# Optimization experiments

Measured on AMD Instinct MI355X. Metric: run time of the kernel, lower is better.

Reference implementation:

```python
import jax, jax.numpy as jnp
import numpy as np
import math

N_HEAD = 16
N_KV_HEAD = 4
N_EMBD = 2048
HEAD_DIM = N_EMBD // N_HEAD  # 128
SCALE = 1.0 / math.sqrt(HEAD_DIM)
B, T = 2, 2048


def setup_inputs() -> dict:
    key = jax.random.key(0)
    ks = jax.random.split(key, 5)
    s = 0.02
    x = jax.random.normal(ks[0], (B, T, N_EMBD), dtype=jnp.float32)
    wq = jax.random.normal(ks[1], (N_EMBD, N_EMBD), dtype=jnp.float32) * s
    wk = jax.random.normal(ks[2], (N_KV_HEAD * HEAD_DIM, N_EMBD), dtype=jnp.float32) * s
    wv = jax.random.normal(ks[3], (N_KV_HEAD * HEAD_DIM, N_EMBD), dtype=jnp.float32) * s
    wo = jax.random.normal(ks[4], (N_EMBD, N_EMBD), dtype=jnp.float32) * s
    return {"x": x, "wq": wq, "wk": wk, "wv": wv, "wo": wo}


def _forward(x, wq, wk, wv, wo):
    b, t, _ = x.shape
    # Linear layers: y = x @ W.T  (torch Linear weight is (out,in))
    q = (x @ wq.T).reshape(b, t, N_HEAD, HEAD_DIM).transpose(0, 2, 1, 3)      # (B,H,T,D)
    k = (x @ wk.T).reshape(b, t, N_KV_HEAD, HEAD_DIM).transpose(0, 2, 1, 3)  # (B,Hkv,T,D)
    v = (x @ wv.T).reshape(b, t, N_KV_HEAD, HEAD_DIM).transpose(0, 2, 1, 3)
    groups = N_HEAD // N_KV_HEAD
    k = jnp.repeat(k, groups, axis=1)  # repeat_interleave over head dim -> (B,H,T,D)
    v = jnp.repeat(v, groups, axis=1)
    # Causal mask: True above diagonal (masked-out positions)
    mask = jnp.triu(jnp.ones((t, t), dtype=bool), k=1)[None, None]  # (1,1,T,T)
    scores = jnp.einsum('bhqd,bhkd->bhqk', q, k) * SCALE
    scores = jnp.where(mask, -jnp.inf, scores)
    attn = jax.nn.softmax(scores, axis=-1)
    attn = jnp.where(mask, 0.0, attn)
    y = jnp.einsum('bhqk,bhkd->bhqd', attn, v)       # (B,H,T,D)
    y = y.transpose(0, 2, 1, 3).reshape(b, t, N_EMBD)
    return y @ wo.T


def reference(x, wq, wk, wv, wo):
    return _forward(x, wq, wk, wv, wo)
```

## Files before the change

### kernel.cpp

```cpp
#include <hip/hip_runtime.h>
#include <cstdint>
#include <cstddef>

typedef __bf16 bf16_t;
typedef __bf16 bf16x8 __attribute__((ext_vector_type(8)));
typedef __bf16 bf16x4 __attribute__((ext_vector_type(4)));
typedef float f32x4 __attribute__((ext_vector_type(4)));

#define GL2LDS16(gptr, lptr)                                                   \
  __builtin_amdgcn_global_load_lds(                                            \
      (__attribute__((address_space(1))) void*)(gptr),                         \
      (__attribute__((address_space(3))) void*)(lptr), 16, 0, 0)

__device__ __forceinline__ float fast_exp2(float x) {
  float r;
  asm volatile("v_exp_f32 %0, %1" : "=v"(r) : "v"(x));
  return r;
}

#define BATCH 2
#define T_SEQ 2048
#define NH 16
#define NKV 4
#define HD 128
#define EMB 2048
#define KVDIM (NKV * HD)
#define MROWS (BATCH * T_SEQ)

__global__ void cvt_all(const float4* __restrict__ x,  const float4* __restrict__ wq,
                        const float4* __restrict__ wk, const float4* __restrict__ wv,
                        const float4* __restrict__ wo,
                        bf16x4* __restrict__ xb,  bf16x4* __restrict__ wqb,
                        bf16x4* __restrict__ wkb, bf16x4* __restrict__ wvb,
                        bf16x4* __restrict__ wob) {
  const int blk = blockIdx.x;
  const float4* src;
  bf16x4* dst;
  int base;
  if (blk < 8192)       { src = x;  dst = xb;  base = blk; }
  else if (blk < 12288) { src = wq; dst = wqb; base = blk - 8192; }
  else if (blk < 13312) { src = wk; dst = wkb; base = blk - 12288; }
  else if (blk < 14336) { src = wv; dst = wvb; base = blk - 13312; }
  else                  { src = wo; dst = wob; base = blk - 14336; }
  const int i = base * 256 + threadIdx.x;
  const float4 v = src[i];
  dst[i] = bf16x4{(__bf16)v.x, (__bf16)v.y, (__bf16)v.z, (__bf16)v.w};
}

#define BK8 64
#define NT8 (EMB / BK8)

__global__ __launch_bounds__(512, 2)
void gemm_qkv8(const bf16_t* __restrict__ A,
               const bf16_t* __restrict__ Wq, const bf16_t* __restrict__ Wk,
               const bf16_t* __restrict__ Wv,
               bf16_t* __restrict__ Qb, bf16_t* __restrict__ Kb,
               bf16_t* __restrict__ Vt, float qalpha)
{
  __shared__ bf16_t lds[2][512 * 64];

  const int tid  = threadIdx.x;
  const int lane = tid & 63;
  const int wv   = tid >> 6;
  const int l15  = lane & 15;
  const int lq   = lane >> 4;

  const int bid0 = blockIdx.x;
  const int bid  = (bid0 & 7) * 24 + (bid0 >> 3);
  const int mt = bid / 12, nt = bid % 12;
  const int m0 = mt * 256;

  const bf16_t* Bmat; int ncol0, seg;
  if (nt < 8)       { Bmat = Wq; ncol0 = nt * 256;        seg = 0; }
  else if (nt < 10) { Bmat = Wk; ncol0 = (nt - 8) * 256;  seg = 1; }
  else              { Bmat = Wv; ncol0 = (nt - 10) * 256; seg = 2; }

  const int wm = (wv >> 2) * 128;
  const int wn = (wv & 3) * 64;

  f32x4 acc[8][4] = {};

  auto stage = [&](int dbuf, int tsrc, int h) {
    const int k0 = tsrc * BK8;
    const bf16_t* src = (h < 2) ? A : Bmat;
    const int rbase = (h < 2) ? (m0 + h * 128) : (ncol0 + (h - 2) * 128);
    bf16_t* dst = &lds[dbuf][h * 8192];
#pragma unroll
    for (int r = 0; r < 2; ++r) {
      const int c = r * 512 + tid;
      const int row = c >> 3, p = c & 7;
      const int sb = p ^ (row & 7);
      GL2LDS16(src + (size_t)(rbase + row) * EMB + k0 + sb * 8, dst + c * 8);
    }
  };

  stage(0, 0, 0); stage(0, 0, 1); stage(0, 0, 2); stage(0, 0, 3);
  stage(1, 1, 2); stage(1, 1, 0); stage(1, 1, 3);
  asm volatile("s_waitcnt vmcnt(6)" ::: "memory");
  __builtin_amdgcn_s_barrier();

  bf16x8 a[4][2], b[4][2];

#pragma unroll 1
  for (int tt = 0; tt < NT8; tt += 2) {
#pragma unroll
    for (int u = 0; u < 2; ++u) {
      const int t   = tt + u;
      const int cur = u;
      const int nxt = u ^ 1;
      const int tn1 = (t + 1 < NT8) ? t + 1 : NT8 - 1;
      const int tn2 = (t + 2 < NT8) ? t + 2 : NT8 - 1;

#pragma unroll
      for (int i = 0; i < 4; ++i) {
        const int row = wm + i * 16 + l15;
#pragma unroll
        for (int ks = 0; ks < 2; ++ks)
          a[i][ks] = *(const bf16x8*)&lds[cur][row * 64 + (((ks * 4 + lq) ^ (row & 7)) * 8)];
      }
#pragma unroll
      for (int j = 0; j < 2; ++j) {
        const int row = 256 + wn + j * 16 + l15;
#pragma unroll
        for (int ks = 0; ks < 2; ++ks)
          b[j][ks] = *(const bf16x8*)&lds[cur][row * 64 + (((ks * 4 + lq) ^ (row & 7)) * 8)];
      }
      stage(nxt, tn1, 1);
      __builtin_amdgcn_s_barrier();
      __builtin_amdgcn_s_setprio(1);
#pragma unroll
      for (int ks = 0; ks < 2; ++ks)
#pragma unroll
        for (int i = 0; i < 4; ++i)
#pragma unroll
          for (int j = 0; j < 2; ++j)
            acc[i][j] = __builtin_amdgcn_mfma_f32_16x16x32_bf16(a[i][ks], b[j][ks], acc[i][j], 0, 0, 0);
      __builtin_amdgcn_s_setprio(0);
      __builtin_amdgcn_s_barrier();

#pragma unroll
      for (int j = 2; j < 4; ++j) {
        const int row = 256 + wn + j * 16 + l15;
#pragma unroll
        for (int ks = 0; ks < 2; ++ks)
          b[j][ks] = *(const bf16x8*)&lds[cur][row * 64 + (((ks * 4 + lq) ^ (row & 7)) * 8)];
      }
      __builtin_amdgcn_s_barrier();
      __builtin_amdgcn_s_setprio(1);
#pragma unroll
      for (int ks = 0; ks < 2; ++ks)
#pragma unroll
        for (int i = 0; i < 4; ++i)
#pragma unroll
          for (int j = 2; j < 4; ++j)
            acc[i][j] = __builtin_amdgcn_mfma_f32_16x16x32_bf16(a[i][ks], b[j][ks], acc[i][j], 0, 0, 0);
      __builtin_amdgcn_s_setprio(0);
      __builtin_amdgcn_s_barrier();

#pragma unroll
      for (int i = 0; i < 4; ++i) {
        const int row = wm + (4 + i) * 16 + l15;
#pragma unroll
        for (int ks = 0; ks < 2; ++ks)
          a[i][ks] = *(const bf16x8*)&lds[cur][row * 64 + (((ks * 4 + lq) ^ (row & 7)) * 8)];
      }
      stage(cur, tn2, 2);
      __builtin_amdgcn_s_barrier();
      __builtin_amdgcn_s_setprio(1);
#pragma unroll
      for (int ks = 0; ks < 2; ++ks)
#pragma unroll
        for (int i = 0; i < 4; ++i)
#pragma unroll
          for (int j = 2; j < 4; ++j)
            acc[4 + i][j] = __builtin_amdgcn_mfma_f32_16x16x32_bf16(a[i][ks], b[j][ks], acc[4 + i][j], 0, 0, 0);
      __builtin_amdgcn_s_setprio(0);
      __builtin_amdgcn_s_barrier();

      stage(cur, tn2, 0);
      stage(cur, tn2, 3);
      __builtin_amdgcn_s_barrier();
      __builtin_amdgcn_s_setprio(1);
#pragma unroll
      for (int ks = 0; ks < 2; ++ks)
#pragma unroll
        for (int i = 0; i < 4; ++i)
#pragma unroll
          for (int j = 0; j < 2; ++j)
            acc[4 + i][j] = __builtin_amdgcn_mfma_f32_16x16x32_bf16(a[i][ks], b[j][ks], acc[4 + i][j], 0, 0, 0);
      __builtin_amdgcn_s_setprio(0);
      asm volatile("s_waitcnt vmcnt(6)" ::: "memory");
      __builtin_amdgcn_s_barrier();
    }
  }
  asm volatile("s_waitcnt vmcnt(0)" ::: "memory");

  if (seg == 0) {
#pragma unroll
    for (int i = 0; i < 8; ++i) {
      const int rbase = m0 + wm + i * 16 + lq * 4;
#pragma unroll
      for (int j = 0; j < 4; ++j) {
        const int col = ncol0 + wn + j * 16 + l15;
#pragma unroll
        for (int r = 0; r < 4; ++r)
          Qb[(size_t)(rbase + r) * EMB + col] = (bf16_t)(acc[i][j][r] * qalpha);
      }
    }
  } else if (seg == 1) {
#pragma unroll
    for (int i = 0; i < 8; ++i) {
      const int rbase = m0 + wm + i * 16 + lq * 4;
#pragma unroll
      for (int j = 0; j < 4; ++j) {
        const int col = ncol0 + wn + j * 16 + l15;
#pragma unroll
        for (int r = 0; r < 4; ++r)
          Kb[(size_t)(rbase + r) * KVDIM + col] = (bf16_t)acc[i][j][r];
      }
    }
  } else {
    const int bb = m0 >> 11;
    const int mloc0 = (m0 & 2047) + wm + lq * 4;
#pragma unroll
    for (int i = 0; i < 8; ++i) {
      const int mloc = mloc0 + i * 16;
#pragma unroll
      for (int j = 0; j < 4; ++j) {
        const int d = ncol0 + wn + j * 16 + l15;
        *(bf16x4*)(Vt + (size_t)(bb * KVDIM + d) * T_SEQ + mloc) =
            bf16x4{(__bf16)acc[i][j][0], (__bf16)acc[i][j][1],
                   (__bf16)acc[i][j][2], (__bf16)acc[i][j][3]};
      }
    }
  }
}

__global__ __launch_bounds__(256, 2)
void gemm_out(const bf16_t* __restrict__ A, const bf16_t* __restrict__ Bm,
              float* __restrict__ C, int M, int N, int K)
{
  __shared__ bf16_t As[128 * 64];
  __shared__ bf16_t Bs[128 * 64];

  const int tid  = threadIdx.x;
  const int lane = tid & 63;
  const int wv   = tid >> 6;
  const int m0 = blockIdx.y * 128;
  const int n0 = blockIdx.x * 128;
  const int wm = (wv >> 1) * 64;
  const int wn = (wv & 1) * 64;
  const int l15 = lane & 15;
  const int lq  = lane >> 4;

  f32x4 acc[4][4] = {};
  const int srow = tid >> 3;
  const int scol = (tid & 7) * 8;

  for (int k0 = 0; k0 < K; k0 += 64) {
#pragma unroll
    for (int r = 0; r < 4; ++r) {
      const int row = r * 32 + srow;
      GL2LDS16(A + (size_t)(m0 + row) * K + k0 + scol, As + row * 64 + scol);
    }
#pragma unroll
    for (int r = 0; r < 4; ++r) {
      const int row = r * 32 + srow;
      GL2LDS16(Bm + (size_t)(n0 + row) * K + k0 + scol, Bs + row * 64 + scol);
    }
    __syncthreads();

#pragma unroll
    for (int ks = 0; ks < 2; ++ks) {
      const int kc = ks * 32 + lq * 8;
      bf16x8 af[4], bf[4];
#pragma unroll
      for (int i = 0; i < 4; ++i)
        af[i] = *(const bf16x8*)(As + (wm + i * 16 + l15) * 64 + kc);
#pragma unroll
      for (int j = 0; j < 4; ++j)
        bf[j] = *(const bf16x8*)(Bs + (wn + j * 16 + l15) * 64 + kc);
#pragma unroll
      for (int i = 0; i < 4; ++i)
#pragma unroll
        for (int j = 0; j < 4; ++j)
          acc[i][j] = __builtin_amdgcn_mfma_f32_16x16x32_bf16(af[i], bf[j], acc[i][j], 0, 0, 0);
    }
    __syncthreads();
  }

#pragma unroll
  for (int i = 0; i < 4; ++i) {
    const int rbase = m0 + wm + i * 16 + lq * 4;
#pragma unroll
    for (int j = 0; j < 4; ++j) {
      const int col = n0 + wn + j * 16 + l15;
#pragma unroll
      for (int r = 0; r < 4; ++r)
        C[(size_t)(rbase + r) * N + col] = acc[i][j][r];
    }
  }
}

#define PSTR 72

__global__ __launch_bounds__(256, 2)
void attn_fwd(const bf16_t* __restrict__ Q, const bf16_t* __restrict__ Kg,
              const bf16_t* __restrict__ Vt, bf16_t* __restrict__ Y)
{
  __shared__ bf16_t Ks[2][64 * 128];
  __shared__ bf16_t Vs[2][128 * 64];
  __shared__ bf16_t Ps[4][16 * PSTR];

  const int tid  = threadIdx.x;
  const int lane = tid & 63;
  const int wv   = tid >> 6;
  const int l15  = lane & 15;
  const int lq   = lane >> 4;
  const int h  = blockIdx.y;
  const int b  = blockIdx.z;
  const int hkv = h >> 2;
  bf16_t* Psw = Ps[wv];

  auto stage = [&](int kt, int bufsel) {
    const int base_t = b * T_SEQ + kt * 64;
#pragma unroll
    for (int r = 0; r < 4; ++r) {
      const int c = r * 256 + tid;
      const int row = c >> 4, p = c & 15;
      const int sb = p ^ (row & 7);
      GL2LDS16(Kg + (size_t)(base_t + row) * KVDIM + hkv * HD + sb * 8,
               &Ks[bufsel][c * 8]);
    }
#pragma unroll
    for (int r = 0; r < 4; ++r) {
      const int c = r * 256 + tid;
      const int row = c >> 3, p = c & 7;
      const int sb = p ^ (row & 7);
      GL2LDS16(Vt + (size_t)(b * KVDIM + hkv * HD + row) * T_SEQ + kt * 64 + sb * 8,
               &Vs[bufsel][c * 8]);
    }
  };

#pragma unroll 1
  for (int ph = 0; ph < 2; ++ph) {
    const int qt = ph ? blockIdx.x : (31 - blockIdx.x);
    const int q0 = qt * 64;
    const int nkt = qt + 1;
    const int qabs = q0 + wv * 16 + l15;

    bf16x8 qf[4];
    {
      const bf16_t* qp = Q + ((size_t)(b * T_SEQ + qabs) * NH + h) * HD + lq * 8;
#pragma unroll
      for (int ds = 0; ds < 4; ++ds)
        qf[ds] = *(const bf16x8*)(qp + ds * 32);
    }

    float l_part = 0.f;
    f32x4 o[8];
#pragma unroll
    for (int nb = 0; nb < 8; ++nb) o[nb] = f32x4{0.f, 0.f, 0.f, 0.f};

    __syncthreads();
    stage(0, 0);

    for (int kt = 0; kt < nkt; ++kt) {
      const int cur = kt & 1;
      __syncthreads();
      if (kt + 1 < nkt) stage(kt + 1, cur ^ 1);

      f32x4 s[4];
#pragma unroll
      for (int nb = 0; nb < 4; ++nb) {
        s[nb] = f32x4{0.f, 0.f, 0.f, 0.f};
        const int row = nb * 16 + l15;
        const int r7  = row & 7;
#pragma unroll
        for (int ds = 0; ds < 4; ++ds) {
          const bf16x8 kf = *(const bf16x8*)&Ks[cur][row * 128 + (((ds * 4 + lq) ^ r7) * 8)];
          s[nb] = __builtin_amdgcn_mfma_f32_16x16x32_bf16(kf, qf[ds], s[nb], 0, 0, 0);
        }
      }

      const bool dia = (kt == nkt - 1);
#pragma unroll
      for (int nb = 0; nb < 4; ++nb) {
        const int kvb = kt * 64 + nb * 16 + lq * 4;
        float p0, p1, p2, p3;
        if (dia) {
          p0 = (kvb + 0 <= qabs) ? fast_exp2(s[nb][0]) : 0.f;
          p1 = (kvb + 1 <= qabs) ? fast_exp2(s[nb][1]) : 0.f;
          p2 = (kvb + 2 <= qabs) ? fast_exp2(s[nb][2]) : 0.f;
          p3 = (kvb + 3 <= qabs) ? fast_exp2(s[nb][3]) : 0.f;
        } else {
          p0 = fast_exp2(s[nb][0]);
          p1 = fast_exp2(s[nb][1]);
          p2 = fast_exp2(s[nb][2]);
          p3 = fast_exp2(s[nb][3]);
        }
        l_part += (p0 + p1) + (p2 + p3);
        *(bf16x4*)(Psw + l15 * PSTR + nb * 16 + lq * 4) =
            bf16x4{(__bf16)p0, (__bf16)p1, (__bf16)p2, (__bf16)p3};
      }

      asm volatile("s_waitcnt lgkmcnt(0)" ::: "memory");

#pragma unroll
      for (int ks = 0; ks < 2; ++ks) {
        const bf16x8 pf = *(const bf16x8*)(Psw + l15 * PSTR + ks * 32 + lq * 8);
#pragma unroll
        for (int nb = 0; nb < 8; ++nb) {
          const int row = nb * 16 + l15;
          const bf16x8 vf = *(const bf16x8*)&Vs[cur][row * 64 + (((ks * 4 + lq) ^ (row & 7)) * 8)];
          o[nb] = __builtin_amdgcn_mfma_f32_16x16x32_bf16(vf, pf, o[nb], 0, 0, 0);
        }
      }
    }

    float lt = l_part;
    lt += __shfl_xor(lt, 16);
    lt += __shfl_xor(lt, 32);
    const float inv = 1.f / lt;
    bf16_t* yp = Y + ((size_t)(b * T_SEQ + qabs) * NH + h) * HD + lq * 4;
#pragma unroll
    for (int nb = 0; nb < 8; ++nb) {
      *(bf16x4*)(yp + nb * 16) = bf16x4{(__bf16)(o[nb][0] * inv), (__bf16)(o[nb][1] * inv),
                                        (__bf16)(o[nb][2] * inv), (__bf16)(o[nb][3] * inv)};
    }
  }
}

extern "C" void kernel_launch(void* const* d_in, const int* in_sizes, int n_in,
                              void* d_out, int out_size, void* d_ws, size_t ws_size,
                              hipStream_t stream) {
  const float* x  = (const float*)d_in[0];
  const float* wq = (const float*)d_in[1];
  const float* wk = (const float*)d_in[2];
  const float* wv = (const float*)d_in[3];
  const float* wo = (const float*)d_in[4];
  float* out = (float*)d_out;

  const size_t n_x  = (size_t)MROWS * EMB;
  const size_t n_wq = (size_t)EMB * EMB;
  const size_t n_wk = (size_t)KVDIM * EMB;

  bf16_t* xb  = (bf16_t*)d_ws;
  bf16_t* wqb = xb  + n_x;
  bf16_t* wkb = wqb + n_wq;
  bf16_t* wvb = wkb + n_wk;
  bf16_t* wob = wvb + n_wk;
  bf16_t* Qb  = wob + n_wq;
  bf16_t* Kb  = Qb + (size_t)MROWS * EMB;
  bf16_t* Vtb = Kb + (size_t)MROWS * KVDIM;
  bf16_t* Yb  = Vtb + (size_t)MROWS * KVDIM;

  dim3 blk(256);

  cvt_all<<<dim3(18432), blk, 0, stream>>>(
      (const float4*)x, (const float4*)wq, (const float4*)wk, (const float4*)wv, (const float4*)wo,
      (bf16x4*)xb, (bf16x4*)wqb, (bf16x4*)wkb, (bf16x4*)wvb, (bf16x4*)wob);

  const float qalpha = 0.08838834764831845f * 1.4426950408889634f;
  gemm_qkv8<<<dim3(192), dim3(512), 0, stream>>>(xb, wqb, wkb, wvb,
                                                 Qb, Kb, Vtb, qalpha);

  attn_fwd<<<dim3(16, NH, BATCH), blk, 0, stream>>>(Qb, Kb, Vtb, Yb);

  gemm_out<<<dim3(EMB / 128, MROWS / 128), blk, 0, stream>>>(Yb, wob, out, MROWS, EMB, EMB);
}
```

Before: 278.9 us.

## Fuse all stages into one persistent kernel with grid-wide atomic barriers

Replaces the four launches (convert, QKV GEMM, attention, output GEMM) with one persistent kernel of 256 blocks that separates the phases with a software grid barrier built on an atomic counter. The goal is to remove launch overhead and inter-kernel gaps. In exchange, occupancy drops to one 512-thread block per CU with a large shared buffer, and the QKV phase uses only 192 of the 256 blocks. The attention and output GEMM work is remapped onto two 256-thread groups per block, and correctness relies on all blocks being resident at once.

```diff
diff --git a/kernel.cpp b/kernel.cpp
--- a/kernel.cpp
+++ b/kernel.cpp
@@ -27,406 +27,442 @@
 #define KVDIM (NKV * HD)
 #define MROWS (BATCH * T_SEQ)
 
-__global__ void cvt_all(const float4* __restrict__ x,  const float4* __restrict__ wq,
-                        const float4* __restrict__ wk, const float4* __restrict__ wv,
-                        const float4* __restrict__ wo,
-                        bf16x4* __restrict__ xb,  bf16x4* __restrict__ wqb,
-                        bf16x4* __restrict__ wkb, bf16x4* __restrict__ wvb,
-                        bf16x4* __restrict__ wob) {
-  const int blk = blockIdx.x;
-  const float4* src;
-  bf16x4* dst;
-  int base;
-  if (blk < 8192)       { src = x;  dst = xb;  base = blk; }
-  else if (blk < 12288) { src = wq; dst = wqb; base = blk - 8192; }
-  else if (blk < 13312) { src = wk; dst = wkb; base = blk - 12288; }
-  else if (blk < 14336) { src = wv; dst = wvb; base = blk - 13312; }
-  else                  { src = wo; dst = wob; base = blk - 14336; }
-  const int i = base * 256 + threadIdx.x;
-  const float4 v = src[i];
-  dst[i] = bf16x4{(__bf16)v.x, (__bf16)v.y, (__bf16)v.z, (__bf16)v.w};
-}
-
 #define BK8 64
 #define NT8 (EMB / BK8)
-
-__global__ __launch_bounds__(512, 2)
-void gemm_qkv8(const bf16_t* __restrict__ A,
-               const bf16_t* __restrict__ Wq, const bf16_t* __restrict__ Wk,
-               const bf16_t* __restrict__ Wv,
-               bf16_t* __restrict__ Qb, bf16_t* __restrict__ Kb,
-               bf16_t* __restrict__ Vt, float qalpha)
+#define PSTR 72
+#define GRIDB 256
+
+#define ATTN_GRP_BYTES 74752
+#define SMEM_BYTES 149504
+
+__device__ __forceinline__ void gbar(unsigned long long* cnt) {
+  __syncthreads();
+  if (threadIdx.x == 0) {
+    unsigned long long old = __hip_atomic_fetch_add(
+        cnt, 1ULL, __ATOMIC_ACQ_REL, __HIP_MEMORY_SCOPE_AGENT);
+    const unsigned long long tgt = (old / GRIDB + 1) * GRIDB;
+    while (__hip_atomic_load(cnt, __ATOMIC_ACQUIRE,
+                             __HIP_MEMORY_SCOPE_AGENT) < tgt)
+      __builtin_amdgcn_s_sleep(2);
+  }
+  __syncthreads();
+}
+
+__global__ __launch_bounds__(512, 1)
+void fused_all(const float* __restrict__ x,  const float* __restrict__ wq,
+               const float* __restrict__ wk, const float* __restrict__ wv,
+               const float* __restrict__ wo, float* __restrict__ out,
+               bf16_t* __restrict__ xb,  bf16_t* __restrict__ wqb,
+               bf16_t* __restrict__ wkb, bf16_t* __restrict__ wvb,
+               bf16_t* __restrict__ wob,
+               bf16_t* __restrict__ Qb,  bf16_t* __restrict__ Kb,
+               bf16_t* __restrict__ Vt,  bf16_t* __restrict__ Yb,
+               unsigned long long* __restrict__ cnt, float qalpha)
 {
-  __shared__ bf16_t lds[2][512 * 64];
-
-  const int tid  = threadIdx.x;
-  const int lane = tid & 63;
-  const int wv   = tid >> 6;
-  const int l15  = lane & 15;
-  const int lq   = lane >> 4;
-
-  const int bid0 = blockIdx.x;
-  const int bid  = (bid0 & 7) * 24 + (bid0 >> 3);
-  const int mt = bid / 12, nt = bid % 12;
-  const int m0 = mt * 256;
-
-  const bf16_t* Bmat; int ncol0, seg;
-  if (nt < 8)       { Bmat = Wq; ncol0 = nt * 256;        seg = 0; }
-  else if (nt < 10) { Bmat = Wk; ncol0 = (nt - 8) * 256;  seg = 1; }
-  else              { Bmat = Wv; ncol0 = (nt - 10) * 256; seg = 2; }
-
-  const int wm = (wv >> 2) * 128;
-  const int wn = (wv & 3) * 64;
-
-  f32x4 acc[8][4] = {};
-
-  auto stage = [&](int dbuf, int tsrc, int h) {
-    const int k0 = tsrc * BK8;
-    const bf16_t* src = (h < 2) ? A : Bmat;
-    const int rbase = (h < 2) ? (m0 + h * 128) : (ncol0 + (h - 2) * 128);
-    bf16_t* dst = &lds[dbuf][h * 8192];
-#pragma unroll
-    for (int r = 0; r < 2; ++r) {
-      const int c = r * 512 + tid;
-      const int row = c >> 3, p = c & 7;
-      const int sb = p ^ (row & 7);
-      GL2LDS16(src + (size_t)(rbase + row) * EMB + k0 + sb * 8, dst + c * 8);
-    }
-  };
-
-  stage(0, 0, 0); stage(0, 0, 1); stage(0, 0, 2); stage(0, 0, 3);
-  stage(1, 1, 2); stage(1, 1, 0); stage(1, 1, 3);
-  asm volatile("s_waitcnt vmcnt(6)" ::: "memory");
-  __builtin_amdgcn_s_barrier();
-
-  bf16x8 a[4][2], b[4][2];
-
-#pragma unroll 1
-  for (int tt = 0; tt < NT8; tt += 2) {
-#pragma unroll
-    for (int u = 0; u < 2; ++u) {
-      const int t   = tt + u;
-      const int cur = u;
-      const int nxt = u ^ 1;
-      const int tn1 = (t + 1 < NT8) ? t + 1 : NT8 - 1;
-      const int tn2 = (t + 2 < NT8) ? t + 2 : NT8 - 1;
-
-#pragma unroll
-      for (int i = 0; i < 4; ++i) {
-        const int row = wm + i * 16 + l15;
-#pragma unroll
-        for (int ks = 0; ks < 2; ++ks)
-          a[i][ks] = *(const bf16x8*)&lds[cur][row * 64 + (((ks * 4 + lq) ^ (row & 7)) * 8)];
-      }
-#pragma unroll
-      for (int j = 0; j < 2; ++j) {
-        const int row = 256 + wn + j * 16 + l15;
-#pragma unroll
-        for (int ks = 0; ks < 2; ++ks)
-          b[j][ks] = *(const bf16x8*)&lds[cur][row * 64 + (((ks * 4 + lq) ^ (row & 7)) * 8)];
-      }
-      stage(nxt, tn1, 1);
-      __builtin_amdgcn_s_barrier();
-      __builtin_amdgcn_s_setprio(1);
-#pragma unroll
-      for (int ks = 0; ks < 2; ++ks)
-#pragma unroll
-        for (int i = 0; i < 4; ++i)
-#pragma unroll
-          for (int j = 0; j < 2; ++j)
-            acc[i][j] = __builtin_amdgcn_mfma_f32_16x16x32_bf16(a[i][ks], b[j][ks], acc[i][j], 0, 0, 0);
-      __builtin_amdgcn_s_setprio(0);
-      __builtin_amdgcn_s_barrier();
-
-#pragma unroll
-      for (int j = 2; j < 4; ++j) {
-        const int row = 256 + wn + j * 16 + l15;
-#pragma unroll
-        for (int ks = 0; ks < 2; ++ks)
-          b[j][ks] = *(const bf16x8*)&lds[cur][row * 64 + (((ks * 4 + lq) ^ (row & 7)) * 8)];
-      }
-      __builtin_amdgcn_s_barrier();
-      __builtin_amdgcn_s_setprio(1);
-#pragma unroll
-      for (int ks = 0; ks < 2; ++ks)
-#pragma unroll
-        for (int i = 0; i < 4; ++i)
-#pragma unroll
-          for (int j = 2; j < 4; ++j)
-            acc[i][j] = __builtin_amdgcn_mfma_f32_16x16x32_bf16(a[i][ks], b[j][ks], acc[i][j], 0, 0, 0);
-      __builtin_amdgcn_s_setprio(0);
-      __builtin_amdgcn_s_barrier();
-
-#pragma unroll
-      for (int i = 0; i < 4; ++i) {
-        const int row = wm + (4 + i) * 16 + l15;
-#pragma unroll
-        for (int ks = 0; ks < 2; ++ks)
-          a[i][ks] = *(const bf16x8*)&lds[cur][row * 64 + (((ks * 4 + lq) ^ (row & 7)) * 8)];
-      }
-      stage(cur, tn2, 2);
-      __builtin_amdgcn_s_barrier();
-      __builtin_amdgcn_s_setprio(1);
-#pragma unroll
-      for (int ks = 0; ks < 2; ++ks)
-#pragma unroll
-        for (int i = 0; i < 4; ++i)
-#pragma unroll
-          for (int j = 2; j < 4; ++j)
-            acc[4 + i][j] = __builtin_amdgcn_mfma_f32_16x16x32_bf16(a[i][ks], b[j][ks], acc[4 + i][j], 0, 0, 0);
-      __builtin_amdgcn_s_setprio(0);
-      __builtin_amdgcn_s_barrier();
-
-      stage(cur, tn2, 0);
-      stage(cur, tn2, 3);
-      __builtin_amdgcn_s_barrier();
-      __builtin_amdgcn_s_setprio(1);
-#pragma unroll
-      for (int ks = 0; ks < 2; ++ks)
-#pragma unroll
-        for (int i = 0; i < 4; ++i)
-#pragma unroll
-          for (int j = 0; j < 2; ++j)
-            acc[4 + i][j] = __builtin_amdgcn_mfma_f32_16x16x32_bf16(a[i][ks], b[j][ks], acc[4 + i][j], 0, 0, 0);
-      __builtin_amdgcn_s_setprio(0);
-      asm volatile("s_waitcnt vmcnt(6)" ::: "memory");
-      __builtin_amdgcn_s_barrier();
+  __shared__ __align__(16) char smem[SMEM_BYTES];
+
+  const int r   = blockIdx.x;
+  const int tid = threadIdx.x;
+
+  {
+    const float4* x4  = (const float4*)x;
+    const float4* wq4 = (const float4*)wq;
+    const float4* wk4 = (const float4*)wk;
+    const float4* wv4 = (const float4*)wv;
+    const float4* wo4 = (const float4*)wo;
+    bf16x4* xb4  = (bf16x4*)xb;
+    bf16x4* wqb4 = (bf16x4*)wqb;
+    bf16x4* wkb4 = (bf16x4*)wkb;
+    bf16x4* wvb4 = (bf16x4*)wvb;
+    bf16x4* wob4 = (bf16x4*)wob;
+    const unsigned gtid = r * 512 + tid;
+    for (unsigned i = gtid; i < 4718592u; i += GRIDB * 512) {
+      const float4* src; bf16x4* dst; unsigned off;
+      if (i < 3145728u) {
+        if (i < 2097152u) { src = x4;  dst = xb4;  off = i; }
+        else              { src = wq4; dst = wqb4; off = i - 2097152u; }
+      } else if (i < 3670016u) {
+        if (i < 3407872u) { src = wk4; dst = wkb4; off = i - 3145728u; }
+        else              { src = wv4; dst = wvb4; off = i - 3407872u; }
+      } else              { src = wo4; dst = wob4; off = i - 3670016u; }
+      const float4 v = src[off];
+      dst[off] = bf16x4{(__bf16)v.x, (__bf16)v.y, (__bf16)v.z, (__bf16)v.w};
     }
   }
-  asm volatile("s_waitcnt vmcnt(0)" ::: "memory");
-
-  if (seg == 0) {
-#pragma unroll
-    for (int i = 0; i < 8; ++i) {
-      const int rbase = m0 + wm + i * 16 + lq * 4;
-#pragma unroll
-      for (int j = 0; j < 4; ++j) {
-        const int col = ncol0 + wn + j * 16 + l15;
-#pragma unroll
-        for (int r = 0; r < 4; ++r)
-          Qb[(size_t)(rbase + r) * EMB + col] = (bf16_t)(acc[i][j][r] * qalpha);
+
+  gbar(cnt);
+
+  if (r < 192) {
+    bf16_t* lds0 = (bf16_t*)smem;
+    bf16_t* lds1 = lds0 + 512 * 64;
+    bf16_t* ldsp[2] = {lds0, lds1};
+
+    const int lane = tid & 63;
+    const int wv_  = tid >> 6;
+    const int l15  = lane & 15;
+    const int lq   = lane >> 4;
+
+    const int bid0 = r;
+    const int bid  = (bid0 & 7) * 24 + (bid0 >> 3);
+    const int mt = bid / 12, nt = bid % 12;
+    const int m0 = mt * 256;
+
+    const bf16_t* Bmat; int ncol0, seg;
+    if (nt < 8)       { Bmat = wqb; ncol0 = nt * 256;        seg = 0; }
+    else if (nt < 10) { Bmat = wkb; ncol0 = (nt - 8) * 256;  seg = 1; }
+    else              { Bmat = wvb; ncol0 = (nt - 10) * 256; seg = 2; }
+
+    const int wm = (wv_ >> 2) * 128;
+    const int wn = (wv_ & 3) * 64;
+
+    f32x4 acc[8][4] = {};
+
+    auto stage = [&](int dbuf, int tsrc, int h) {
+      const int k0 = tsrc * BK8;
+      const bf16_t* src = (h < 2) ? xb : Bmat;
+      const int rbase = (h < 2) ? (m0 + h * 128) : (ncol0 + (h - 2) * 128);
+      bf16_t* dst = ldsp[dbuf] + h * 8192;
+#pragma unroll
+      for (int rr = 0; rr < 2; ++rr) {
+        const int c = rr * 512 + tid;
+        const int row = c >> 3, p = c & 7;
+        const int sb = p ^ (row & 7);
+        GL2LDS16(src + (size_t)(rbase + row) * EMB + k0 + sb * 8, dst + c * 8);
+      }
+    };
+
+    stage(0, 0, 0); stage(0, 0, 1); stage(0, 0, 2); stage(0, 0, 3);
+    stage(1, 1, 2); stage(1, 1, 0); stage(1, 1, 3);
+    asm volatile("s_waitcnt vmcnt(6)" ::: "memory");
+    __builtin_amdgcn_s_barrier();
+
+    bf16x8 a[4][2], b[4][2];
+
+#pragma unroll 1
+    for (int tt = 0; tt < NT8; tt += 2) {
+#pragma unroll
+      for (int u = 0; u < 2; ++u) {
+        const int t   = tt + u;
+        const int cur = u;
+        const int nxt = u ^ 1;
+        const int tn1 = (t + 1 < NT8) ? t + 1 : NT8 - 1;
+        const int tn2 = (t + 2 < NT8) ? t + 2 : NT8 - 1;
+
+#pragma unroll
+        for (int i = 0; i < 4; ++i) {
+          const int row = wm + i * 16 + l15;
+#pragma unroll
+          for (int ks = 0; ks < 2; ++ks)
+            a[i][ks] = *(const bf16x8*)&ldsp[cur][row * 64 + (((ks * 4 + lq) ^ (row & 7)) * 8)];
+        }
+#pragma unroll
+        for (int j = 0; j < 2; ++j) {
+          const int row = 256 + wn + j * 16 + l15;
+#pragma unroll
+          for (int ks = 0; ks < 2; ++ks)
+            b[j][ks] = *(const bf16x8*)&ldsp[cur][row * 64 + (((ks * 4 + lq) ^ (row & 7)) * 8)];
+        }
+        stage(nxt, tn1, 1);
+        __builtin_amdgcn_s_barrier();
+        __builtin_amdgcn_s_setprio(1);
+#pragma unroll
+        for (int ks = 0; ks < 2; ++ks)
+#pragma unroll
+          for (int i = 0; i < 4; ++i)
+#pragma unroll
+            for (int j = 0; j < 2; ++j)
+              acc[i][j] = __builtin_amdgcn_mfma_f32_16x16x32_bf16(a[i][ks], b[j][ks], acc[i][j], 0, 0, 0);
+        __builtin_amdgcn_s_setprio(0);
+        __builtin_amdgcn_s_barrier();
+
+#pragma unroll
+        for (int j = 2; j < 4; ++j) {
+          const int row = 256 + wn + j * 16 + l15;
+#pragma unroll
+          for (int ks = 0; ks < 2; ++ks)
+            b[j][ks] = *(const bf16x8*)&ldsp[cur][row * 64 + (((ks * 4 + lq) ^ (row & 7)) * 8)];
+        }
+        __builtin_amdgcn_s_barrier();
+        __builtin_amdgcn_s_setprio(1);
+#pragma unroll
+        for (int ks = 0; ks < 2; ++ks)
+#pragma unroll
+          for (int i = 0; i < 4; ++i)
+#pragma unroll
+            for (int j = 2; j < 4; ++j)
+              acc[i][j] = __builtin_amdgcn_mfma_f32_16x16x32_bf16(a[i][ks], b[j][ks], acc[i][j], 0, 0, 0);
+        __builtin_amdgcn_s_setprio(0);
+        __builtin_amdgcn_s_barrier();
+
+#pragma unroll
+        for (int i = 0; i < 4; ++i) {
+          const int row = wm + (4 + i) * 16 + l15;
+#pragma unroll
+          for (int ks = 0; ks < 2; ++ks)
+            a[i][ks] = *(const bf16x8*)&ldsp[cur][row * 64 + (((ks * 4 + lq) ^ (row & 7)) * 8)];
+        }
+        stage(cur, tn2, 2);
+        __builtin_amdgcn_s_barrier();
+        __builtin_amdgcn_s_setprio(1);
+#pragma unroll
+        for (int ks = 0; ks < 2; ++ks)
+#pragma unroll
+          for (int i = 0; i < 4; ++i)
+#pragma unroll
+            for (int j = 2; j < 4; ++j)
+              acc[4 + i][j] = __builtin_amdgcn_mfma_f32_16x16x32_bf16(a[i][ks], b[j][ks], acc[4 + i][j], 0, 0, 0);
+        __builtin_amdgcn_s_setprio(0);
+        __builtin_amdgcn_s_barrier();
+
+        stage(cur, tn2, 0);
+        stage(cur, tn2, 3);
+        __builtin_amdgcn_s_barrier();
+        __builtin_amdgcn_s_setprio(1);
+#pragma unroll
+        for (int ks = 0; ks < 2; ++ks)
+#pragma unroll
+          for (int i = 0; i < 4; ++i)
+#pragma unroll
+            for (int j = 0; j < 2; ++j)
+              acc[4 + i][j] = __builtin_amdgcn_mfma_f32_16x16x32_bf16(a[i][ks], b[j][ks], acc[4 + i][j], 0, 0, 0);
+        __builtin_amdgcn_s_setprio(0);
+        asm volatile("s_waitcnt vmcnt(6)" ::: "memory");
+        __builtin_amdgcn_s_barrier();
       }
     }
-  } else if (seg == 1) {
-#pragma unroll
-    for (int i = 0; i < 8; ++i) {
-      const int rbase = m0 + wm + i * 16 + lq * 4;
-#pragma unroll
-      for (int j = 0; j < 4; ++j) {
-        const int col = ncol0 + wn + j * 16 + l15;
-#pragma unroll
-        for (int r = 0; r < 4; ++r)
-          Kb[(size_t)(rbase + r) * KVDIM + col] = (bf16_t)acc[i][j][r];
-      }
-    }
-  } else {
-    const int bb = m0 >> 11;
-    const int mloc0 = (m0 & 2047) + wm + lq * 4;
-#pragma unroll
-    for (int i = 0; i < 8; ++i) {
-      const int mloc = mloc0 + i * 16;
-#pragma unroll
-      for (int j = 0; j < 4; ++j) {
-        const int d = ncol0 + wn + j * 16 + l15;
-        *(bf16x4*)(Vt + (size_t)(bb * KVDIM + d) * T_SEQ + mloc) =
-            bf16x4{(__bf16)acc[i][j][0], (__bf16)acc[i][j][1],
-                   (__bf16)acc[i][j][2], (__bf16)acc[i][j][3]};
+    asm volatile("s_waitcnt vmcnt(0)" ::: "memory");
+
+    if (seg == 0) {
+#pragma unroll
+      for (int i = 0; i < 8; ++i) {
+        const int rbase = m0 + wm + i * 16 + lq * 4;
+#pragma unroll
+        for (int j = 0; j < 4; ++j) {
+          const int col = ncol0 + wn + j * 16 + l15;
+#pragma unroll
+          for (int rr = 0; rr < 4; ++rr)
+            Qb[(size_t)(rbase + rr) * EMB + col] = (bf16_t)(acc[i][j][rr] * qalpha);
+        }
+      }
+    } else if (seg == 1) {
+#pragma unroll
+      for (int i = 0; i < 8; ++i) {
+        const int rbase = m0 + wm + i * 16 + lq * 4;
+#pragma unroll
+        for (int j = 0; j < 4; ++j) {
+          const int col = ncol0 + wn + j * 16 + l15;
+#pragma unroll
+          for (int rr = 0; rr < 4; ++rr)
+            Kb[(size_t)(rbase + rr) * KVDIM + col] = (bf16_t)acc[i][j][rr];
+        }
+      }
+    } else {
+      const int bb = m0 >> 11;
+      const int mloc0 = (m0 & 2047) + wm + lq * 4;
+#pragma unroll
+      for (int i = 0; i < 8; ++i) {
+        const int mloc = mloc0 + i * 16;
+#pragma unroll
+        for (int j = 0; j < 4; ++j) {
+          const int d = ncol0 + wn + j * 16 + l15;
+          *(bf16x4*)(Vt + (size_t)(bb * KVDIM + d) * T_SEQ + mloc) =
+              bf16x4{(__bf16)acc[i][j][0], (__bf16)acc[i][j][1],
+                     (__bf16)acc[i][j][2], (__bf16)acc[i][j][3]};
+        }
       }
     }
   }
-}
-
-__global__ __launch_bounds__(256, 2)
-void gemm_out(const bf16_t* __restrict__ A, const bf16_t* __restrict__ Bm,
-              float* __restrict__ C, int M, int N, int K)
-{
-  __shared__ bf16_t As[128 * 64];
-  __shared__ bf16_t Bs[128 * 64];
-
-  const int tid  = threadIdx.x;
-  const int lane = tid & 63;
-  const int wv   = tid >> 6;
-  const int m0 = blockIdx.y * 128;
-  const int n0 = blockIdx.x * 128;
-  const int wm = (wv >> 1) * 64;
-  const int wn = (wv & 1) * 64;
-  const int l15 = lane & 15;
-  const int lq  = lane >> 4;
-
-  f32x4 acc[4][4] = {};
-  const int srow = tid >> 3;
-  const int scol = (tid & 7) * 8;
-
-  for (int k0 = 0; k0 < K; k0 += 64) {
-#pragma unroll
-    for (int r = 0; r < 4; ++r) {
-      const int row = r * 32 + srow;
-      GL2LDS16(A + (size_t)(m0 + row) * K + k0 + scol, As + row * 64 + scol);
-    }
-#pragma unroll
-    for (int r = 0; r < 4; ++r) {
-      const int row = r * 32 + srow;
-      GL2LDS16(Bm + (size_t)(n0 + row) * K + k0 + scol, Bs + row * 64 + scol);
-    }
-    __syncthreads();
-
-#pragma unroll
-    for (int ks = 0; ks < 2; ++ks) {
-      const int kc = ks * 32 + lq * 8;
-      bf16x8 af[4], bf[4];
-#pragma unroll
-      for (int i = 0; i < 4; ++i)
-        af[i] = *(const bf16x8*)(As + (wm + i * 16 + l15) * 64 + kc);
-#pragma unroll
-      for (int j = 0; j < 4; ++j)
-        bf[j] = *(const bf16x8*)(Bs + (wn + j * 16 + l15) * 64 + kc);
-#pragma unroll
-      for (int i = 0; i < 4; ++i)
-#pragma unroll
-        for (int j = 0; j < 4; ++j)
-          acc[i][j] = __builtin_amdgcn_mfma_f32_16x16x32_bf16(af[i], bf[j], acc[i][j], 0, 0, 0);
-    }
-    __syncthreads();
-  }
-
-#pragma unroll
-  for (int i = 0; i < 4; ++i) {
-    const int rbase = m0 + wm + i * 16 + lq * 4;
-#pragma unroll
-    for (int j = 0; j < 4; ++j) {
-      const int col = n0 + wn + j * 16 + l15;
-#pragma unroll
-      for (int r = 0; r < 4; ++r)
-        C[(size_t)(rbase + r) * N + col] = acc[i][j][r];
+
+  gbar(cnt);
+
+  {
+    const int grp = tid >> 8;
+    const int tg  = tid & 255;
+    const int lane = tg & 63;
+    const int wv_  = tg >> 6;
+    const int l15  = lane & 15;
+    const int lq   = lane >> 4;
+    const int xq = r & 15;
+    const int h  = r >> 4;
+    const int b  = grp;
+    const int hkv = h >> 2;
+
+    bf16_t* Ksg = (bf16_t*)(smem + grp * ATTN_GRP_BYTES);
+    bf16_t* Vsg = Ksg + 2 * 8192;
+    bf16_t* Psw = Vsg + 2 * 8192 + wv_ * 16 * PSTR;
+
+    auto stage = [&](int kt, int bufsel) {
+      const int base_t = b * T_SEQ + kt * 64;
+#pragma unroll
+      for (int rr = 0; rr < 4; ++rr) {
+        const int c = rr * 256 + tg;
+        const int row = c >> 4, p = c & 15;
+        const int sb = p ^ (row & 7);
+        GL2LDS16(Kb + (size_t)(base_t + row) * KVDIM + hkv * HD + sb * 8,
+                 Ksg + bufsel * 8192 + c * 8);
+      }
+#pragma unroll
+      for (int rr = 0; rr < 4; ++rr) {
+        const int c = rr * 256 + tg;
+        const int row = c >> 3, p = c & 7;
+        const int sb = p ^ (row & 7);
+        GL2LDS16(Vt + (size_t)(b * KVDIM + hkv * HD + row) * T_SEQ + kt * 64 + sb * 8,
+                 Vsg + bufsel * 8192 + c * 8);
+      }
+    };
+
+#pragma unroll 1
+    for (int ph = 0; ph < 2; ++ph) {
+      const int qt = ph ? xq : (31 - xq);
+      const int nkt = qt + 1;
+      const int qabs = qt * 64 + wv_ * 16 + l15;
+
+      bf16x8 qf[4];
+      {
+        const bf16_t* qp = Qb + ((size_t)(b * T_SEQ + qabs) * NH + h) * HD + lq * 8;
+#pragma unroll
+        for (int ds = 0; ds < 4; ++ds)
+          qf[ds] = *(const bf16x8*)(qp + ds * 32);
+      }
+
+      float l_part = 0.f;
+      f32x4 o[8];
+#pragma unroll
+      for (int nb = 0; nb < 8; ++nb) o[nb] = f32x4{0.f, 0.f, 0.f, 0.f};
+
+      __syncthreads();
+      stage(0, 0);
+
+      for (int kt = 0; kt < nkt; ++kt) {
+        const int cur = kt & 1;
+        __syncthreads();
+        if (kt + 1 < nkt) stage(kt + 1, cur ^ 1);
+
+        f32x4 s[4];
+#pragma unroll
+        for (int nb = 0; nb < 4; ++nb) {
+          s[nb] = f32x4{0.f, 0.f, 0.f, 0.f};
+          const int row = nb * 16 + l15;
+          const int r7  = row & 7;
+#pragma unroll
+          for (int ds = 0; ds < 4; ++ds) {
+            const bf16x8 kf = *(const bf16x8*)&Ksg[cur * 8192 + row * 128 + (((ds * 4 + lq) ^ r7) * 8)];
+            s[nb] = __builtin_amdgcn_mfma_f32_16x16x32_bf16(kf, qf[ds], s[nb], 0, 0, 0);
+          }
+        }
+
+        const bool dia = (kt == nkt - 1);
+#pragma unroll
+        for (int nb = 0; nb < 4; ++nb) {
+          const int kvb = kt * 64 + nb * 16 + lq * 4;
+          float p0, p1, p2, p3;
+          if (dia) {
+            p0 = (kvb + 0 <= qabs) ? fast_exp2(s[nb][0]) : 0.f;
+            p1 = (kvb + 1 <= qabs) ? fast_exp2(s[nb][1]) : 0.f;
+            p2 = (kvb + 2 <= qabs) ? fast_exp2(s[nb][2]) : 0.f;
+            p3 = (kvb + 3 <= qabs) ? fast_exp2(s[nb][3]) : 0.f;
+          } else {
+            p0 = fast_exp2(s[nb][0]);
+            p1 = fast_exp2(s[nb][1]);
+            p2 = fast_exp2(s[nb][2]);
+            p3 = fast_exp2(s[nb][3]);
+          }
+          l_part += (p0 + p1) + (p2 + p3);
+          *(bf16x4*)(Psw + l15 * PSTR + nb * 16 + lq * 4) =
+              bf16x4{(__bf16)p0, (__bf16)p1, (__bf16)p2, (__bf16)p3};
+        }
+
+        asm volatile("s_waitcnt lgkmcnt(0)" ::: "memory");
+
+#pragma unroll
+        for (int ks = 0; ks < 2; ++ks) {
+          const bf16x8 pf = *(const bf16x8*)(Psw + l15 * PSTR + ks * 32 + lq * 8);
+#pragma unroll
+          for (int nb = 0; nb < 8; ++nb) {
+            const int row = nb * 16 + l15;
+            const bf16x8 vf = *(const bf16x8*)&Vsg[cur * 8192 + row * 64 + (((ks * 4 + lq) ^ (row & 7)) * 8)];
+            o[nb] = __builtin_amdgcn_mfma_f32_16x16x32_bf16(vf, pf, o[nb], 0, 0, 0);
+          }
+        }
+      }
+
+      float lt = l_part;
+      lt += __shfl_xor(lt, 16);
+      lt += __shfl_xor(lt, 32);
+      const float inv = 1.f / lt;
+      bf16_t* yp = Yb + ((size_t)(b * T_SEQ + qabs) * NH + h) * HD + lq * 4;
+#pragma unroll
+      for (int nb = 0; nb < 8; ++nb) {
+        *(bf16x4*)(yp + nb * 16) = bf16x4{(__bf16)(o[nb][0] * inv), (__bf16)(o[nb][1] * inv),
+                                          (__bf16)(o[nb][2] * inv), (__bf16)(o[nb][3] * inv)};
+      }
     }
   }
-}
-
-#define PSTR 72
-
-__global__ __launch_bounds__(256, 2)
-void attn_fwd(const bf16_t* __restrict__ Q, const bf16_t* __restrict__ Kg,
-              const bf16_t* __restrict__ Vt, bf16_t* __restrict__ Y)
-{
-  __shared__ bf16_t Ks[2][64 * 128];
-  __shared__ bf16_t Vs[2][128 * 64];
-  __shared__ bf16_t Ps[4][16 * PSTR];
-
-  const int tid  = threadIdx.x;
-  const int lane = tid & 63;
-  const int wv   = tid >> 6;
-  const int l15  = lane & 15;
-  const int lq   = lane >> 4;
-  const int h  = blockIdx.y;
-  const int b  = blockIdx.z;
-  const int hkv = h >> 2;
-  bf16_t* Psw = Ps[wv];
-
-  auto stage = [&](int kt, int bufsel) {
-    const int base_t = b * T_SEQ + kt * 64;
-#pragma unroll
-    for (int r = 0; r < 4; ++r) {
-      const int c = r * 256 + tid;
-      const int row = c >> 4, p = c & 15;
-      const int sb = p ^ (row & 7);
-      GL2LDS16(Kg + (size_t)(base_t + row) * KVDIM + hkv * HD + sb * 8,
-               &Ks[bufsel][c * 8]);
+
+  gbar(cnt);
+
+  {
+    const int grp = tid >> 8;
+    const int tg  = tid & 255;
+    const int lane = tg & 63;
+    const int wv_  = tg >> 6;
+    const int v = r * 2 + grp;
+    const int m0 = (v >> 4) * 128;
+    const int n0 = (v & 15) * 128;
+    const int wm = (wv_ >> 1) * 64;
+    const int wn = (wv_ & 1) * 64;
+    const int l15 = lane & 15;
+    const int lq  = lane >> 4;
+
+    bf16_t* As = (bf16_t*)(smem + grp * 32768);
+    bf16_t* Bs = As + 128 * 64;
+
+    f32x4 acc[4][4] = {};
+    const int srow = tg >> 3;
+    const int scol = (tg & 7) * 8;
+
+    for (int k0 = 0; k0 < EMB; k0 += 64) {
+#pragma unroll
+      for (int rr = 0; rr < 4; ++rr) {
+        const int row = rr * 32 + srow;
+        GL2LDS16(Yb + (size_t)(m0 + row) * EMB + k0 + scol, As + row * 64 + scol);
+      }
+#pragma unroll
+      for (int rr = 0; rr < 4; ++rr) {
+        const int row = rr * 32 + srow;
+        GL2LDS16(wob + (size_t)(n0 + row) * EMB + k0 + scol, Bs + row * 64 + scol);
+      }
+      __syncthreads();
+
+#pragma unroll
+      for (int ks = 0; ks < 2; ++ks) {
+        const int kc = ks * 32 + lq * 8;
+        bf16x8 af[4], bf[4];
+#pragma unroll
+        for (int i = 0; i < 4; ++i)
+          af[i] = *(const bf16x8*)(As + (wm + i * 16 + l15) * 64 + kc);
+#pragma unroll
+        for (int j = 0; j < 4; ++j)
+          bf[j] = *(const bf16x8*)(Bs + (wn + j * 16 + l15) * 64 + kc);
+#pragma unroll
+        for (int i = 0; i < 4; ++i)
+#pragma unroll
+          for (int j = 0; j < 4; ++j)
+            acc[i][j] = __builtin_amdgcn_mfma_f32_16x16x32_bf16(af[i], bf[j], acc[i][j], 0, 0, 0);
+      }
+      __syncthreads();
     }
-#pragma unroll
-    for (int r = 0; r < 4; ++r) {
-      const int c = r * 256 + tid;
-      const int row = c >> 3, p = c & 7;
-      const int sb = p ^ (row & 7);
-      GL2LDS16(Vt + (size_t)(b * KVDIM + hkv * HD + row) * T_SEQ + kt * 64 + sb * 8,
-               &Vs[bufsel][c * 8]);
-    }
-  };
-
-#pragma unroll 1
-  for (int ph = 0; ph < 2; ++ph) {
-    const int qt = ph ? blockIdx.x : (31 - blockIdx.x);
-    const int q0 = qt * 64;
-    const int nkt = qt + 1;
-    const int qabs = q0 + wv * 16 + l15;
-
-    bf16x8 qf[4];
-    {
-      const bf16_t* qp = Q + ((size_t)(b * T_SEQ + qabs) * NH + h) * HD + lq * 8;
-#pragma unroll
-      for (int ds = 0; ds < 4; ++ds)
-        qf[ds] = *(const bf16x8*)(qp + ds * 32);
-    }
-
-    float l_part = 0.f;
-    f32x4 o[8];
-#pragma unroll
-    for (int nb = 0; nb < 8; ++nb) o[nb] = f32x4{0.f, 0.f, 0.f, 0.f};
-
-    __syncthreads();
-    stage(0, 0);
-
-    for (int kt = 0; kt < nkt; ++kt) {
-      const int cur = kt & 1;
-      __syncthreads();
-      if (kt + 1 < nkt) stage(kt + 1, cur ^ 1);
-
-      f32x4 s[4];
-#pragma unroll
-      for (int nb = 0; nb < 4; ++nb) {
-        s[nb] = f32x4{0.f, 0.f, 0.f, 0.f};
-        const int row = nb * 16 + l15;
-        const int r7  = row & 7;
-#pragma unroll
-        for (int ds = 0; ds < 4; ++ds) {
-          const bf16x8 kf = *(const bf16x8*)&Ks[cur][row * 128 + (((ds * 4 + lq) ^ r7) * 8)];
-          s[nb] = __builtin_amdgcn_mfma_f32_16x16x32_bf16(kf, qf[ds], s[nb], 0, 0, 0);
-        }
-      }
-
-      const bool dia = (kt == nkt - 1);
-#pragma unroll
-      for (int nb = 0; nb < 4; ++nb) {
-        const int kvb = kt * 64 + nb * 16 + lq * 4;
-        float p0, p1, p2, p3;
-        if (dia) {
-          p0 = (kvb + 0 <= qabs) ? fast_exp2(s[nb][0]) : 0.f;
-          p1 = (kvb + 1 <= qabs) ? fast_exp2(s[nb][1]) : 0.f;
-          p2 = (kvb + 2 <= qabs) ? fast_exp2(s[nb][2]) : 0.f;
-          p3 = (kvb + 3 <= qabs) ? fast_exp2(s[nb][3]) : 0.f;
-        } else {
-          p0 = fast_exp2(s[nb][0]);
-          p1 = fast_exp2(s[nb][1]);
-          p2 = fast_exp2(s[nb][2]);
-          p3 = fast_exp2(s[nb][3]);
-        }
-        l_part += (p0 + p1) + (p2 + p3);
-        *(bf16x4*)(Psw + l15 * PSTR + nb * 16 + lq * 4) =
-            bf16x4{(__bf16)p0, (__bf16)p1, (__bf16)p2, (__bf16)p3};
-      }
-
-      asm volatile("s_waitcnt lgkmcnt(0)" ::: "memory");
-
-#pragma unroll
-      for (int ks = 0; ks < 2; ++ks) {
-        const bf16x8 pf = *(const bf16x8*)(Psw + l15 * PSTR + ks * 32 + lq * 8);
-#pragma unroll
-        for (int nb = 0; nb < 8; ++nb) {
-          const int row = nb * 16 + l15;
-          const bf16x8 vf = *(const bf16x8*)&Vs[cur][row * 64 + (((ks * 4 + lq) ^ (row & 7)) * 8)];
-          o[nb] = __builtin_amdgcn_mfma_f32_16x16x32_bf16(vf, pf, o[nb], 0, 0, 0);
-        }
-      }
-    }
-
-    float lt = l_part;
-    lt += __shfl_xor(lt, 16);
-    lt += __shfl_xor(lt, 32);
-    const float inv = 1.f / lt;
-    bf16_t* yp = Y + ((size_t)(b * T_SEQ + qabs) * NH + h) * HD + lq * 4;
-#pragma unroll
-    for (int nb = 0; nb < 8; ++nb) {
-      *(bf16x4*)(yp + nb * 16) = bf16x4{(__bf16)(o[nb][0] * inv), (__bf16)(o[nb][1] * inv),
-                                        (__bf16)(o[nb][2] * inv), (__bf16)(o[nb][3] * inv)};
+
+#pragma unroll
+    for (int i = 0; i < 4; ++i) {
+      const int rbase = m0 + wm + i * 16 + lq * 4;
+#pragma unroll
+      for (int j = 0; j < 4; ++j) {
+        const int col = n0 + wn + j * 16 + l15;
+#pragma unroll
+        for (int rr = 0; rr < 4; ++rr)
+          out[(size_t)(rbase + rr) * EMB + col] = acc[i][j][rr];
+      }
     }
   }
 }
@@ -445,7 +481,8 @@
   const size_t n_wq = (size_t)EMB * EMB;
   const size_t n_wk = (size_t)KVDIM * EMB;
 
-  bf16_t* xb  = (bf16_t*)d_ws;
+  unsigned long long* cnt = (unsigned long long*)d_ws;
+  bf16_t* xb  = (bf16_t*)((char*)d_ws + 16);
   bf16_t* wqb = xb  + n_x;
   bf16_t* wkb = wqb + n_wq;
   bf16_t* wvb = wkb + n_wk;
@@ -455,17 +492,10 @@
   bf16_t* Vtb = Kb + (size_t)MROWS * KVDIM;
   bf16_t* Yb  = Vtb + (size_t)MROWS * KVDIM;
 
-  dim3 blk(256);
-
-  cvt_all<<<dim3(18432), blk, 0, stream>>>(
-      (const float4*)x, (const float4*)wq, (const float4*)wk, (const float4*)wv, (const float4*)wo,
-      (bf16x4*)xb, (bf16x4*)wqb, (bf16x4*)wkb, (bf16x4*)wvb, (bf16x4*)wob);
+  hipMemsetAsync(cnt, 0, 8, stream);
 
   const float qalpha = 0.08838834764831845f * 1.4426950408889634f;
-  gemm_qkv8<<<dim3(192), dim3(512), 0, stream>>>(xb, wqb, wkb, wvb,
-                                                 Qb, Kb, Vtb, qalpha);
-
-  attn_fwd<<<dim3(16, NH, BATCH), blk, 0, stream>>>(Qb, Kb, Vtb, Yb);
-
-  gemm_out<<<dim3(EMB / 128, MROWS / 128), blk, 0, stream>>>(Yb, wob, out, MROWS, EMB, EMB);
+  fused_all<<<dim3(GRIDB), dim3(512), 0, stream>>>(
+      x, wq, wk, wv, wo, out,
+      xb, wqb, wkb, wvb, wob, Qb, Kb, Vtb, Yb, cnt, qalpha);
 }
```

New measurement: 571.1 us. 2.05x slower.
